# Performance work log

Measured on AMD Instinct MI355X. Metric: run time of the kernel, lower is better.

Reference implementation:

```python
import jax, jax.numpy as jnp
import numpy as np

B, L, D, H = 2, 2048, 1024, 16
HD = D // H  # head_dim = 64


def setup_inputs() -> dict:
    key = jax.random.key(0)
    ks = jax.random.split(key, 9)
    s = 0.02
    return {
        "x": jax.random.normal(ks[0], (B, L, D), dtype=jnp.float32),
        "wq": jax.random.normal(ks[1], (D, D), dtype=jnp.float32) * s,
        "bq": jnp.zeros((D,), dtype=jnp.float32),
        "wk": jax.random.normal(ks[2], (D, D), dtype=jnp.float32) * s,
        "bk": jnp.zeros((D,), dtype=jnp.float32),
        "wv": jax.random.normal(ks[3], (D, D), dtype=jnp.float32) * s,
        "bv": jnp.zeros((D,), dtype=jnp.float32),
        "wo": jax.random.normal(ks[4], (D, D), dtype=jnp.float32) * s,
        "bo": jnp.zeros((D,), dtype=jnp.float32),
    }


def reference(x, wq, bq, wk, bk, wv, bv, wo, bo):
    b, l, d = x.shape
    # projections -> [B, H, L, HD]
    def split_heads(t):
        return t.reshape(b, l, H, HD).transpose(0, 2, 1, 3)
    q = split_heads(x @ wq + bq)
    k = split_heads(x @ wk + bk)
    v = split_heads(x @ wv + bv)
    scores = jnp.einsum('bhqd,bhkd->bhqk', q, k) / jnp.sqrt(jnp.float32(HD))
    # causal mask via -inf then clamp to [-50, 50]: masked entries become -50 (faithful to torch code)
    mask = jnp.triu(jnp.full((l, l), -jnp.inf, dtype=scores.dtype), k=1)
    scores = jnp.clip(scores + mask[None, None, :, :], -50.0, 50.0)
    attn = jax.nn.softmax(scores, axis=-1)
    # dropout is identity in eval/deterministic mode
    out = jnp.einsum('bhqk,bhkd->bhqd', attn, v)
    out = out.transpose(0, 2, 1, 3).reshape(b, l, d)
    out = out @ wo + bo
    return out, attn
```

## Files before the change

kernel.cpp:

```cpp
#include <hip/hip_runtime.h>
#include <hip/hip_bf16.h>

#define B_  2
#define L_  2048
#define D_  1024
#define H_  16
#define HD_ 64

typedef __bf16 bf16x8 __attribute__((ext_vector_type(8)));
typedef float  f32x4  __attribute__((ext_vector_type(4)));
using bf16_t = __hip_bfloat16;

static __device__ __forceinline__ f32x4 mfma16(bf16x8 a, bf16x8 b, f32x4 c) {
    return __builtin_amdgcn_mfma_f32_16x16x32_bf16(a, b, c, 0, 0, 0);
}

static __device__ __forceinline__ void gl16(const bf16_t* g, bf16_t* l) {
    __builtin_amdgcn_global_load_lds(
        (const __attribute__((address_space(1))) unsigned int*)g,
        (__attribute__((address_space(3))) unsigned int*)l, 16, 0, 0);
}

__global__ __launch_bounds__(256) void k_convert(const float* __restrict__ in,
                                                 bf16_t* __restrict__ out, int n8) {
    int idx = blockIdx.x * 256 + threadIdx.x;
    if (idx >= n8) return;
    const float4* p = (const float4*)in + (size_t)idx * 2;
    float4 a = p[0], b = p[1];
    union { bf16_t h[8]; bf16x8 v; } u;
    u.h[0] = __float2bfloat16(a.x); u.h[1] = __float2bfloat16(a.y);
    u.h[2] = __float2bfloat16(a.z); u.h[3] = __float2bfloat16(a.w);
    u.h[4] = __float2bfloat16(b.x); u.h[5] = __float2bfloat16(b.y);
    u.h[6] = __float2bfloat16(b.z); u.h[7] = __float2bfloat16(b.w);
    *(bf16x8*)(out + (size_t)idx * 8) = u.v;
}

__global__ __launch_bounds__(256) void k_transpose4(
        const float* __restrict__ w0, const float* __restrict__ w1,
        const float* __restrict__ w2, const float* __restrict__ w3,
        bf16_t* __restrict__ t0, bf16_t* __restrict__ t1,
        bf16_t* __restrict__ t2, bf16_t* __restrict__ t3) {
    __shared__ bf16_t tile[64][65];
    int z = blockIdx.z;
    const float* w = (z == 0) ? w0 : (z == 1) ? w1 : (z == 2) ? w2 : w3;
    bf16_t* wt     = (z == 0) ? t0 : (z == 1) ? t1 : (z == 2) ? t2 : t3;
    int t  = threadIdx.x;
    int kb = blockIdx.x * 64, nb = blockIdx.y * 64;
    int r  = t >> 4, c4 = (t & 15) * 4;
    #pragma unroll
    for (int it = 0; it < 4; ++it) {
        int kr = r + it * 16;
        float4 v = *(const float4*)&w[(size_t)(kb + kr) * D_ + nb + c4];
        tile[kr][c4 + 0] = __float2bfloat16(v.x);
        tile[kr][c4 + 1] = __float2bfloat16(v.y);
        tile[kr][c4 + 2] = __float2bfloat16(v.z);
        tile[kr][c4 + 3] = __float2bfloat16(v.w);
    }
    __syncthreads();
    #pragma unroll
    for (int it = 0; it < 4; ++it) {
        int nr = r + it * 16;
        union { bf16_t h[4]; unsigned long long u; } o;
        o.h[0] = tile[c4 + 0][nr];
        o.h[1] = tile[c4 + 1][nr];
        o.h[2] = tile[c4 + 2][nr];
        o.h[3] = tile[c4 + 3][nr];
        *(unsigned long long*)&wt[(size_t)(nb + nr) * D_ + kb + c4] = o.u;
    }
}

__global__ __launch_bounds__(256, 3) void k_gemm_qkv(
        const bf16_t* __restrict__ A,
        const bf16_t* __restrict__ Wq, const bf16_t* __restrict__ Wk, const bf16_t* __restrict__ Wv,
        const float* __restrict__ bq, const float* __restrict__ bk, const float* __restrict__ bv,
        bf16_t* __restrict__ Qo, bf16_t* __restrict__ Ko, bf16_t* __restrict__ Vo) {
    __shared__ __align__(16) bf16_t Al[128][32];
    __shared__ __align__(16) bf16_t Bl[128][32];
    const int K = D_;
    int z = blockIdx.z;
    const bf16_t* Wt = (z == 0) ? Wq : (z == 1) ? Wk : Wv;
    const float* bias = (z == 0) ? bq : (z == 1) ? bk : bv;
    bf16_t* outp      = (z == 0) ? Qo : (z == 1) ? Ko : Vo;
    int tid = threadIdx.x, lane = tid & 63, wid = tid >> 6;
    int m0 = blockIdx.y * 128, n0 = blockIdx.x * 128;
    int wm = (wid >> 1) * 64, wn = (wid & 1) * 64;
    int r16 = lane & 15, g = lane >> 4;
    int lrow = lane >> 2, lcol = (lane & 3) * 8;
    f32x4 acc[4][4] = {};
    for (int kb = 0; kb < K; kb += 32) {
        __syncthreads();
        gl16(&A [(size_t)(m0 + wid * 32 + lrow) * K + kb + lcol],      &Al[wid * 32][0]);
        gl16(&A [(size_t)(m0 + wid * 32 + 16 + lrow) * K + kb + lcol], &Al[wid * 32 + 16][0]);
        gl16(&Wt[(size_t)(n0 + wid * 32 + lrow) * K + kb + lcol],      &Bl[wid * 32][0]);
        gl16(&Wt[(size_t)(n0 + wid * 32 + 16 + lrow) * K + kb + lcol], &Bl[wid * 32 + 16][0]);
        __syncthreads();
        bf16x8 af[4], bfr[4];
        #pragma unroll
        for (int i = 0; i < 4; ++i) af[i]  = *(const bf16x8*)&Al[wm + i * 16 + r16][g * 8];
        #pragma unroll
        for (int j = 0; j < 4; ++j) bfr[j] = *(const bf16x8*)&Bl[wn + j * 16 + r16][g * 8];
        #pragma unroll
        for (int i = 0; i < 4; ++i)
            #pragma unroll
            for (int j = 0; j < 4; ++j)
                acc[i][j] = mfma16(af[i], bfr[j], acc[i][j]);
    }
    #pragma unroll
    for (int i = 0; i < 4; ++i) {
        #pragma unroll
        for (int j = 0; j < 4; ++j) {
            int n = n0 + wn + j * 16 + r16;
            float bv2 = bias[n];
            #pragma unroll
            for (int e = 0; e < 4; ++e) {
                int m = m0 + wm + i * 16 + g * 4 + e;
                float v = acc[i][j][e] + bv2;
                int b = m >> 11, l = m & (L_ - 1);
                int h = n >> 6, hd = n & 63;
                if (z != 2)
                    outp[(((size_t)(b * H_ + h)) * L_ + l) * HD_ + hd] = __float2bfloat16(v);
                else
                    outp[(((size_t)(b * H_ + h)) * HD_ + hd) * L_ + l] = __float2bfloat16(v);
            }
        }
    }
}

__global__ __launch_bounds__(256, 2) void k_gemm_o(const bf16_t* __restrict__ A,
                                                   const bf16_t* __restrict__ Wt,
                                                   const float* __restrict__ bias,
                                                   float* __restrict__ outp) {
    __shared__ __align__(16) bf16_t Al[128][32];
    __shared__ __align__(16) bf16_t Bl[64][32];
    const int K = D_;
    int tid = threadIdx.x, lane = tid & 63, wid = tid >> 6;
    int m0 = blockIdx.y * 128, n0 = blockIdx.x * 64;
    int wm = (wid >> 1) * 64, wn = (wid & 1) * 32;
    int r16 = lane & 15, g = lane >> 4;
    int lrow = lane >> 2, lcol = (lane & 3) * 8;
    f32x4 acc[4][2] = {};
    for (int kb = 0; kb < K; kb += 32) {
        __syncthreads();
        gl16(&A [(size_t)(m0 + wid * 32 + lrow) * K + kb + lcol],      &Al[wid * 32][0]);
        gl16(&A [(size_t)(m0 + wid * 32 + 16 + lrow) * K + kb + lcol], &Al[wid * 32 + 16][0]);
        gl16(&Wt[(size_t)(n0 + wid * 16 + lrow) * K + kb + lcol],      &Bl[wid * 16][0]);
        __syncthreads();
        bf16x8 af[4], bfr[2];
        #pragma unroll
        for (int i = 0; i < 4; ++i) af[i]  = *(const bf16x8*)&Al[wm + i * 16 + r16][g * 8];
        #pragma unroll
        for (int j = 0; j < 2; ++j) bfr[j] = *(const bf16x8*)&Bl[wn + j * 16 + r16][g * 8];
        #pragma unroll
        for (int i = 0; i < 4; ++i)
            #pragma unroll
            for (int j = 0; j < 2; ++j)
                acc[i][j] = mfma16(af[i], bfr[j], acc[i][j]);
    }
    #pragma unroll
    for (int i = 0; i < 4; ++i)
        #pragma unroll
        for (int j = 0; j < 2; ++j) {
            int n = n0 + wn + j * 16 + r16;
            float bv = bias[n];
            #pragma unroll
            for (int e = 0; e < 4; ++e) {
                int m = m0 + wm + i * 16 + g * 4 + e;
                outp[(size_t)m * D_ + n] = acc[i][j][e] + bv;
            }
        }
}

__global__ __launch_bounds__(128, 3) void k_attn(const bf16_t* __restrict__ Q,
                                                 const bf16_t* __restrict__ Kb,
                                                 const bf16_t* __restrict__ VT,
                                                 bf16_t* __restrict__ ctx,
                                                 float* __restrict__ attn) {
    __shared__ __align__(16) bf16_t K_lds[2][32][64];
    __shared__ __align__(16) bf16_t V_lds[2][64][32];
    __shared__ __align__(16) char   pbuf[2][4608];

    int tid = threadIdx.x, lane = tid & 63, wid = tid >> 6;
    int bid = blockIdx.x;
    int j   = bid >> 3;
    int bh  = (bid & 7) + 8 * (j & 3);
    int qt64 = 31 - (j >> 2);
    int b = bh >> 4, h = bh & 15;
    int qb = qt64 * 64;
    const int diag = 2 * qt64 + 1;
    const bf16_t* Qh = Q  + (size_t)bh * L_ * HD_;
    const bf16_t* Kh = Kb + (size_t)bh * L_ * HD_;
    const bf16_t* Vh = VT + (size_t)bh * HD_ * L_;
    int r16 = lane & 15, g = lane >> 4;
    const float scale2 = 0.125f * 1.44269504088896340736f;
    const float clamp2 = 50.0f * 1.44269504088896340736f;

    bf16_t (*plds)[40] = (bf16_t(*)[40])pbuf[wid];
    float  (*pf32)[36] = (float (*)[36])pbuf[wid];

    int qrow0 = qb + wid * 32;

    bf16x8 q[2][2];
    #pragma unroll
    for (int p = 0; p < 2; ++p)
        #pragma unroll
        for (int hh = 0; hh < 2; ++hh)
            q[p][hh] = *(const bf16x8*)&Qh[(qrow0 + p * 16 + r16) * HD_ + hh * 32 + g * 8];

    int l = lane;
    int krow = l >> 3, kch = (l & 7) ^ (l >> 3);
    int vrow = l >> 2, vch = l & 3;
    auto STAGE_K = [&](int kt1, int nxt) {
        #pragma unroll
        for (int i = 0; i < 2; ++i) {
            int ii = wid * 2 + i;
            gl16(&Kh[(size_t)(kt1 * 32 + 8 * ii + krow) * 64 + kch * 8], &K_lds[nxt][8 * ii][0]);
        }
    };
    auto STAGE_V = [&](int kt1, int nxt) {
        #pragma unroll
        for (int i = 0; i < 2; ++i) {
            int ii = wid * 2 + i;
            gl16(&Vh[(size_t)(16 * ii + vrow) * L_ + kt1 * 32 + vch * 8], &V_lds[nxt][16 * ii][0]);
        }
    };

    f32x4 ctxa[2][4] = {};
    float zsum[2] = {0.f, 0.f};

    STAGE_K(0, 0); STAGE_V(0, 0);
    int cur = 0;
    for (int kt = 0; kt <= diag; ++kt) {
        __syncthreads();
        int nxt = cur ^ 1;
        if (kt < diag) { STAGE_K(kt + 1, nxt); STAGE_V(kt + 1, nxt); }
        bf16x8 kf[2][2], vf[4];
        #pragma unroll
        for (int s = 0; s < 2; ++s)
            #pragma unroll
            for (int hh = 0; hh < 2; ++hh)
                kf[s][hh] = *(const bf16x8*)&K_lds[cur][s * 16 + r16][((hh * 4 + g) ^ (r16 & 7)) * 8];
        #pragma unroll
        for (int t = 0; t < 4; ++t)
            vf[t] = *(const bf16x8*)&V_lds[cur][t * 16 + r16][g * 8];
        f32x4 sa[2][2];
        #pragma unroll
        for (int p = 0; p < 2; ++p)
            #pragma unroll
            for (int s = 0; s < 2; ++s) {
                f32x4 zz = {};
                sa[p][s] = mfma16(kf[s][1], q[p][1], mfma16(kf[s][0], q[p][0], zz));
            }
        int kb = kt * 32;
        #pragma unroll
        for (int p = 0; p < 2; ++p) {
            int qrow = qrow0 + p * 16 + r16;
            #pragma unroll
            for (int s = 0; s < 2; ++s) {
                union { bf16_t hv[4]; unsigned long long u; } pk;
                #pragma unroll
                for (int e = 0; e < 4; ++e) {
                    int key = kb + s * 16 + g * 4 + e;
                    float sc = sa[p][s][e] * scale2;
                    sc = fminf(fmaxf(sc, -clamp2), clamp2);
                    float ev = (key > qrow) ? 0.f : exp2f(sc);
                    zsum[p] += ev;
                    pk.hv[e] = __float2bfloat16(ev);
                }
                *(unsigned long long*)&plds[p * 16 + r16][s * 16 + g * 4] = pk.u;
            }
        }
        #pragma unroll
        for (int p = 0; p < 2; ++p) {
            bf16x8 pa = *(const bf16x8*)&plds[p * 16 + r16][g * 8];
            #pragma unroll
            for (int t = 0; t < 4; ++t)
                ctxa[p][t] = mfma16(pa, vf[t], ctxa[p][t]);
        }
        cur = nxt;
    }

    float invz[2];
    #pragma unroll
    for (int p = 0; p < 2; ++p) {
        float v = zsum[p];
        v += __shfl_xor(v, 16);
        v += __shfl_xor(v, 32);
        invz[p] = 1.f / v;
    }

    #pragma unroll
    for (int p = 0; p < 2; ++p) {
        #pragma unroll
        for (int e = 0; e < 4; ++e) {
            float izq = __shfl(invz[p], g * 4 + e);
            int qrow = qrow0 + p * 16 + g * 4 + e;
            #pragma unroll
            for (int t = 0; t < 4; ++t) {
                int col = h * HD_ + t * 16 + r16;
                ctx[((size_t)b * L_ + qrow) * D_ + col] =
                    __float2bfloat16(ctxa[p][t][e] * izq);
            }
        }
    }

    __syncthreads();
    STAGE_K(0, 0);
    cur = 0;
    for (int kt = 0; kt <= diag; ++kt) {
        __syncthreads();
        int nxt = cur ^ 1;
        if (kt < diag) STAGE_K(kt + 1, nxt);
        bf16x8 kf[2][2];
        #pragma unroll
        for (int s = 0; s < 2; ++s)
            #pragma unroll
            for (int hh = 0; hh < 2; ++hh)
                kf[s][hh] = *(const bf16x8*)&K_lds[cur][s * 16 + r16][((hh * 4 + g) ^ (r16 & 7)) * 8];
        f32x4 sa[2][2];
        #pragma unroll
        for (int p = 0; p < 2; ++p)
            #pragma unroll
            for (int s = 0; s < 2; ++s) {
                f32x4 zz = {};
                sa[p][s] = mfma16(kf[s][1], q[p][1], mfma16(kf[s][0], q[p][0], zz));
            }
        int kb = kt * 32;
        #pragma unroll
        for (int p = 0; p < 2; ++p) {
            int qrow = qrow0 + p * 16 + r16;
            #pragma unroll
            for (int s = 0; s < 2; ++s) {
                float4 fv;
                float* fp = &fv.x;
                #pragma unroll
                for (int e = 0; e < 4; ++e) {
                    int key = kb + s * 16 + g * 4 + e;
                    float sc = sa[p][s][e] * scale2;
                    sc = fminf(fmaxf(sc, -clamp2), clamp2);
                    fp[e] = (key > qrow) ? 0.f : exp2f(sc) * invz[p];
                }
                *(float4*)&pf32[p * 16 + r16][s * 16 + g * 4] = fv;
            }
        }
        #pragma unroll
        for (int jj = 0; jj < 4; ++jj) {
            int row = jj * 8 + (lane >> 3);
            float4 t = *(const float4*)&pf32[row][(lane & 7) * 4];
            *(float4*)&attn[((size_t)bh * L_ + qrow0 + row) * L_ + kb + (lane & 7) * 4] = t;
        }
        cur = nxt;
    }

    int zs = qb + 64;
    if (zs < L_) {
        float4 z4 = make_float4(0.f, 0.f, 0.f, 0.f);
        for (int r = 0; r < 32; ++r) {
            float* rowp = attn + ((size_t)bh * L_ + qrow0 + r) * L_;
            for (int c = zs + lane * 4; c < L_; c += 256)
                *(float4*)&rowp[c] = z4;
        }
    }
}

extern "C" void kernel_launch(void* const* d_in, const int* in_sizes, int n_in,
                              void* d_out, int out_size, void* d_ws, size_t ws_size,
                              hipStream_t stream) {
    const float* x  = (const float*)d_in[0];
    const float* wq = (const float*)d_in[1];
    const float* bq = (const float*)d_in[2];
    const float* wk = (const float*)d_in[3];
    const float* bk = (const float*)d_in[4];
    const float* wv = (const float*)d_in[5];
    const float* bv = (const float*)d_in[6];
    const float* wo = (const float*)d_in[7];
    const float* bo = (const float*)d_in[8];

    char* ws = (char*)d_ws;
    bf16_t* xb   = (bf16_t*)(ws);
    bf16_t* wqt  = (bf16_t*)(ws + ( 8u << 20));
    bf16_t* wkt  = (bf16_t*)(ws + (10u << 20));
    bf16_t* wvt  = (bf16_t*)(ws + (12u << 20));
    bf16_t* wot  = (bf16_t*)(ws + (14u << 20));
    bf16_t* Qb   = (bf16_t*)(ws + (16u << 20));
    bf16_t* Kbuf = (bf16_t*)(ws + (24u << 20));
    bf16_t* VTb  = (bf16_t*)(ws + (32u << 20));
    bf16_t* ctxb = (bf16_t*)(ws + (40u << 20));

    float* out  = (float*)d_out;
    float* attn = out + (size_t)B_ * L_ * D_;

    k_convert<<<2048, 256, 0, stream>>>(x, xb, (B_ * L_ * D_) / 8);
    dim3 tg4(16, 16, 4);
    k_transpose4<<<tg4, 256, 0, stream>>>(wq, wk, wv, wo, wqt, wkt, wvt, wot);

    dim3 g3(D_ / 128, (B_ * L_) / 128, 3);
    k_gemm_qkv<<<g3, 256, 0, stream>>>(xb, wqt, wkt, wvt, bq, bk, bv, Qb, Kbuf, VTb);

    k_attn<<<1024, 128, 0, stream>>>(Qb, Kbuf, VTb, ctxb, attn);

    dim3 gg(D_ / 64, (B_ * L_) / 128);
    k_gemm_o<<<gg, 256, 0, stream>>>(ctxb, wot, bo, (float*)d_out);
}
```

Measured before the change: 262.3 us.

## Restructure attention to 4-wave blocks with 64-key tiles and register-held P

Merges the x conversion and the weight transposes into one prep launch. Restructures the attention kernel so each block runs 4 waves of 16 query rows over 64-key K/V tiles. The softmax probabilities are packed into bf16 MFMA operands in registers with v_cvt_pk_bf16_f32, so they no longer go through an LDS scratch buffer. The V tile is swizzled to avoid bank conflicts, and attn rows are written straight from registers instead of being restaged through LDS. This cuts LDS traffic and barriers per tile, but the global stores of attn are less coalesced.

```diff
diff --git a/kernel.cpp b/kernel.cpp
--- a/kernel.cpp
+++ b/kernel.cpp
@@ -10,6 +10,8 @@
 typedef __bf16 bf16x8 __attribute__((ext_vector_type(8)));
 typedef float  f32x4  __attribute__((ext_vector_type(4)));
 using bf16_t = __hip_bfloat16;
+typedef unsigned int u32;
+typedef unsigned long long u64;
 
 static __device__ __forceinline__ f32x4 mfma16(bf16x8 a, bf16x8 b, f32x4 c) {
     return __builtin_amdgcn_mfma_f32_16x16x32_bf16(a, b, c, 0, 0, 0);
@@ -21,30 +23,38 @@
         (__attribute__((address_space(3))) unsigned int*)l, 16, 0, 0);
 }
 
-__global__ __launch_bounds__(256) void k_convert(const float* __restrict__ in,
-                                                 bf16_t* __restrict__ out, int n8) {
-    int idx = blockIdx.x * 256 + threadIdx.x;
-    if (idx >= n8) return;
-    const float4* p = (const float4*)in + (size_t)idx * 2;
-    float4 a = p[0], b = p[1];
-    union { bf16_t h[8]; bf16x8 v; } u;
-    u.h[0] = __float2bfloat16(a.x); u.h[1] = __float2bfloat16(a.y);
-    u.h[2] = __float2bfloat16(a.z); u.h[3] = __float2bfloat16(a.w);
-    u.h[4] = __float2bfloat16(b.x); u.h[5] = __float2bfloat16(b.y);
-    u.h[6] = __float2bfloat16(b.z); u.h[7] = __float2bfloat16(b.w);
-    *(bf16x8*)(out + (size_t)idx * 8) = u.v;
-}
-
-__global__ __launch_bounds__(256) void k_transpose4(
+static __device__ __forceinline__ u32 cvtpk(float lo, float hi) {
+    u32 r;
+    asm("v_cvt_pk_bf16_f32 %0, %1, %2" : "=v"(r) : "v"(lo), "v"(hi));
+    return r;
+}
+
+__global__ __launch_bounds__(256) void k_prep(
+        const float* __restrict__ x,
         const float* __restrict__ w0, const float* __restrict__ w1,
         const float* __restrict__ w2, const float* __restrict__ w3,
+        bf16_t* __restrict__ xb,
         bf16_t* __restrict__ t0, bf16_t* __restrict__ t1,
         bf16_t* __restrict__ t2, bf16_t* __restrict__ t3) {
     __shared__ bf16_t tile[64][65];
     int z = blockIdx.z;
+    int t = threadIdx.x;
+    if (z >= 4) {
+        int slice = z - 4;
+        int lin = blockIdx.y * 16 + blockIdx.x;
+        int idx = (slice * 256 + lin) * 256 + t;
+        const float4* p = (const float4*)x + (size_t)idx * 2;
+        float4 a = p[0], b = p[1];
+        union { bf16_t h[8]; bf16x8 v; } u;
+        u.h[0] = __float2bfloat16(a.x); u.h[1] = __float2bfloat16(a.y);
+        u.h[2] = __float2bfloat16(a.z); u.h[3] = __float2bfloat16(a.w);
+        u.h[4] = __float2bfloat16(b.x); u.h[5] = __float2bfloat16(b.y);
+        u.h[6] = __float2bfloat16(b.z); u.h[7] = __float2bfloat16(b.w);
+        *(bf16x8*)(xb + (size_t)idx * 8) = u.v;
+        return;
+    }
     const float* w = (z == 0) ? w0 : (z == 1) ? w1 : (z == 2) ? w2 : w3;
     bf16_t* wt     = (z == 0) ? t0 : (z == 1) ? t1 : (z == 2) ? t2 : t3;
-    int t  = threadIdx.x;
     int kb = blockIdx.x * 64, nb = blockIdx.y * 64;
     int r  = t >> 4, c4 = (t & 15) * 4;
     #pragma unroll
@@ -60,12 +70,12 @@
     #pragma unroll
     for (int it = 0; it < 4; ++it) {
         int nr = r + it * 16;
-        union { bf16_t h[4]; unsigned long long u; } o;
+        union { bf16_t h[4]; u64 u; } o;
         o.h[0] = tile[c4 + 0][nr];
         o.h[1] = tile[c4 + 1][nr];
         o.h[2] = tile[c4 + 2][nr];
         o.h[3] = tile[c4 + 3][nr];
-        *(unsigned long long*)&wt[(size_t)(nb + nr) * D_ + kb + c4] = o.u;
+        *(u64*)&wt[(size_t)(nb + nr) * D_ + kb + c4] = o.u;
     }
 }
 
@@ -170,62 +180,52 @@
         }
 }
 
-__global__ __launch_bounds__(128, 3) void k_attn(const bf16_t* __restrict__ Q,
+__global__ __launch_bounds__(256, 4) void k_attn(const bf16_t* __restrict__ Q,
                                                  const bf16_t* __restrict__ Kb,
                                                  const bf16_t* __restrict__ VT,
                                                  bf16_t* __restrict__ ctx,
                                                  float* __restrict__ attn) {
-    __shared__ __align__(16) bf16_t K_lds[2][32][64];
-    __shared__ __align__(16) bf16_t V_lds[2][64][32];
-    __shared__ __align__(16) char   pbuf[2][4608];
-
+    __shared__ __align__(16) bf16_t K_lds[2][64][64];
+    __shared__ __align__(16) bf16_t V_lds[2][64][64];
     int tid = threadIdx.x, lane = tid & 63, wid = tid >> 6;
     int bid = blockIdx.x;
-    int j   = bid >> 3;
-    int bh  = (bid & 7) + 8 * (j & 3);
-    int qt64 = 31 - (j >> 2);
+    int idx = bid >> 3;
+    int bh  = (bid & 7) + 8 * (idx & 3);
+    int qt  = 31 - (idx >> 2);
     int b = bh >> 4, h = bh & 15;
-    int qb = qt64 * 64;
-    const int diag = 2 * qt64 + 1;
+    int qb = qt * 64;
+    const int diag = qt;
     const bf16_t* Qh = Q  + (size_t)bh * L_ * HD_;
     const bf16_t* Kh = Kb + (size_t)bh * L_ * HD_;
     const bf16_t* Vh = VT + (size_t)bh * HD_ * L_;
     int r16 = lane & 15, g = lane >> 4;
     const float scale2 = 0.125f * 1.44269504088896340736f;
     const float clamp2 = 50.0f * 1.44269504088896340736f;
-
-    bf16_t (*plds)[40] = (bf16_t(*)[40])pbuf[wid];
-    float  (*pf32)[36] = (float (*)[36])pbuf[wid];
-
-    int qrow0 = qb + wid * 32;
-
-    bf16x8 q[2][2];
-    #pragma unroll
-    for (int p = 0; p < 2; ++p)
-        #pragma unroll
-        for (int hh = 0; hh < 2; ++hh)
-            q[p][hh] = *(const bf16x8*)&Qh[(qrow0 + p * 16 + r16) * HD_ + hh * 32 + g * 8];
-
-    int l = lane;
-    int krow = l >> 3, kch = (l & 7) ^ (l >> 3);
-    int vrow = l >> 2, vch = l & 3;
+    int qrow0 = qb + wid * 16;
+    int qrow  = qrow0 + r16;
+
+    bf16x8 q0 = *(const bf16x8*)&Qh[(size_t)(qrow0 + r16) * HD_ + g * 8];
+    bf16x8 q1 = *(const bf16x8*)&Qh[(size_t)(qrow0 + r16) * HD_ + 32 + g * 8];
+
+    int srow = lane >> 3, sunit = ((lane & 7) ^ (lane >> 3)) * 8;
     auto STAGE_K = [&](int kt1, int nxt) {
         #pragma unroll
         for (int i = 0; i < 2; ++i) {
-            int ii = wid * 2 + i;
-            gl16(&Kh[(size_t)(kt1 * 32 + 8 * ii + krow) * 64 + kch * 8], &K_lds[nxt][8 * ii][0]);
+            int cb = wid * 16 + i * 8;
+            gl16(&Kh[(size_t)(kt1 * 64 + cb + srow) * HD_ + sunit], &K_lds[nxt][cb][0]);
         }
     };
     auto STAGE_V = [&](int kt1, int nxt) {
         #pragma unroll
         for (int i = 0; i < 2; ++i) {
-            int ii = wid * 2 + i;
-            gl16(&Vh[(size_t)(16 * ii + vrow) * L_ + kt1 * 32 + vch * 8], &V_lds[nxt][16 * ii][0]);
+            int cb = wid * 16 + i * 8;
+            gl16(&Vh[(size_t)(cb + srow) * L_ + kt1 * 64 + sunit], &V_lds[nxt][cb][0]);
         }
     };
 
-    f32x4 ctxa[2][4] = {};
-    float zsum[2] = {0.f, 0.f};
+    f32x4 ctxa[4] = {};
+    float zsum = 0.f;
+    int rx = r16 & 7;
 
     STAGE_K(0, 0); STAGE_V(0, 0);
     int cur = 0;
@@ -233,128 +233,101 @@
         __syncthreads();
         int nxt = cur ^ 1;
         if (kt < diag) { STAGE_K(kt + 1, nxt); STAGE_V(kt + 1, nxt); }
-        bf16x8 kf[2][2], vf[4];
-        #pragma unroll
-        for (int s = 0; s < 2; ++s)
-            #pragma unroll
-            for (int hh = 0; hh < 2; ++hh)
-                kf[s][hh] = *(const bf16x8*)&K_lds[cur][s * 16 + r16][((hh * 4 + g) ^ (r16 & 7)) * 8];
-        #pragma unroll
-        for (int t = 0; t < 4; ++t)
-            vf[t] = *(const bf16x8*)&V_lds[cur][t * 16 + r16][g * 8];
-        f32x4 sa[2][2];
-        #pragma unroll
-        for (int p = 0; p < 2; ++p)
-            #pragma unroll
-            for (int s = 0; s < 2; ++s) {
+        int kb = kt * 64;
+        #pragma unroll
+        for (int sub = 0; sub < 2; ++sub) {
+            f32x4 sa[2];
+            #pragma unroll
+            for (int sp = 0; sp < 2; ++sp) {
+                int krow = sub * 32 + sp * 16 + r16;
+                bf16x8 kf0 = *(const bf16x8*)&K_lds[cur][krow][(g ^ rx) * 8];
+                bf16x8 kf1 = *(const bf16x8*)&K_lds[cur][krow][((4 + g) ^ rx) * 8];
                 f32x4 zz = {};
-                sa[p][s] = mfma16(kf[s][1], q[p][1], mfma16(kf[s][0], q[p][0], zz));
-            }
-        int kb = kt * 32;
-        #pragma unroll
-        for (int p = 0; p < 2; ++p) {
-            int qrow = qrow0 + p * 16 + r16;
-            #pragma unroll
-            for (int s = 0; s < 2; ++s) {
-                union { bf16_t hv[4]; unsigned long long u; } pk;
+                sa[sp] = mfma16(kf1, q1, mfma16(kf0, q0, zz));
+            }
+            int kb2 = kb + sub * 32;
+            u32 dw[2][2];
+            #pragma unroll
+            for (int sp = 0; sp < 2; ++sp) {
+                float ev[4];
                 #pragma unroll
                 for (int e = 0; e < 4; ++e) {
-                    int key = kb + s * 16 + g * 4 + e;
-                    float sc = sa[p][s][e] * scale2;
-                    sc = fminf(fmaxf(sc, -clamp2), clamp2);
-                    float ev = (key > qrow) ? 0.f : exp2f(sc);
-                    zsum[p] += ev;
-                    pk.hv[e] = __float2bfloat16(ev);
+                    int key = kb2 + sp * 16 + g * 4 + e;
+                    float sc = fminf(fmaxf(sa[sp][e] * scale2, -clamp2), clamp2);
+                    ev[e] = (key > qrow) ? 0.f : exp2f(sc);
+                    zsum += ev[e];
                 }
-                *(unsigned long long*)&plds[p * 16 + r16][s * 16 + g * 4] = pk.u;
-            }
-        }
-        #pragma unroll
-        for (int p = 0; p < 2; ++p) {
-            bf16x8 pa = *(const bf16x8*)&plds[p * 16 + r16][g * 8];
-            #pragma unroll
-            for (int t = 0; t < 4; ++t)
-                ctxa[p][t] = mfma16(pa, vf[t], ctxa[p][t]);
+                dw[sp][0] = cvtpk(ev[0], ev[1]);
+                dw[sp][1] = cvtpk(ev[2], ev[3]);
+            }
+            union { u32 u[4]; bf16x8 v; } pa;
+            pa.u[0] = dw[0][0]; pa.u[1] = dw[0][1];
+            pa.u[2] = dw[1][0]; pa.u[3] = dw[1][1];
+            #pragma unroll
+            for (int t = 0; t < 4; ++t) {
+                int vrow = t * 16 + r16;
+                int u0 = ((sub * 4 + (g >> 1)) ^ rx) * 8 + (g & 1) * 4;
+                int u1 = ((sub * 4 + 2 + (g >> 1)) ^ rx) * 8 + (g & 1) * 4;
+                union { u64 d[2]; bf16x8 v; } vf;
+                vf.d[0] = *(const u64*)&V_lds[cur][vrow][u0];
+                vf.d[1] = *(const u64*)&V_lds[cur][vrow][u1];
+                ctxa[t] = mfma16(pa.v, vf.v, ctxa[t]);
+            }
         }
         cur = nxt;
-    }
-
-    float invz[2];
-    #pragma unroll
-    for (int p = 0; p < 2; ++p) {
-        float v = zsum[p];
-        v += __shfl_xor(v, 16);
-        v += __shfl_xor(v, 32);
-        invz[p] = 1.f / v;
-    }
-
-    #pragma unroll
-    for (int p = 0; p < 2; ++p) {
-        #pragma unroll
-        for (int e = 0; e < 4; ++e) {
-            float izq = __shfl(invz[p], g * 4 + e);
-            int qrow = qrow0 + p * 16 + g * 4 + e;
-            #pragma unroll
-            for (int t = 0; t < 4; ++t) {
-                int col = h * HD_ + t * 16 + r16;
-                ctx[((size_t)b * L_ + qrow) * D_ + col] =
-                    __float2bfloat16(ctxa[p][t][e] * izq);
-            }
-        }
     }
 
     __syncthreads();
     STAGE_K(0, 0);
+
+    float v = zsum;
+    v += __shfl_xor(v, 16);
+    v += __shfl_xor(v, 32);
+    float invz = 1.f / v;
+
+    #pragma unroll
+    for (int e = 0; e < 4; ++e) {
+        float izq = __shfl(invz, g * 4 + e);
+        int qr = qrow0 + g * 4 + e;
+        #pragma unroll
+        for (int t = 0; t < 4; ++t)
+            ctx[((size_t)b * L_ + qr) * D_ + h * HD_ + t * 16 + r16] =
+                __float2bfloat16(ctxa[t][e] * izq);
+    }
+
     cur = 0;
     for (int kt = 0; kt <= diag; ++kt) {
         __syncthreads();
         int nxt = cur ^ 1;
         if (kt < diag) STAGE_K(kt + 1, nxt);
-        bf16x8 kf[2][2];
-        #pragma unroll
-        for (int s = 0; s < 2; ++s)
-            #pragma unroll
-            for (int hh = 0; hh < 2; ++hh)
-                kf[s][hh] = *(const bf16x8*)&K_lds[cur][s * 16 + r16][((hh * 4 + g) ^ (r16 & 7)) * 8];
-        f32x4 sa[2][2];
-        #pragma unroll
-        for (int p = 0; p < 2; ++p)
-            #pragma unroll
-            for (int s = 0; s < 2; ++s) {
+        int kb = kt * 64;
+        #pragma unroll
+        for (int sub = 0; sub < 2; ++sub)
+            #pragma unroll
+            for (int sp = 0; sp < 2; ++sp) {
+                int krow = sub * 32 + sp * 16 + r16;
+                bf16x8 kf0 = *(const bf16x8*)&K_lds[cur][krow][(g ^ rx) * 8];
+                bf16x8 kf1 = *(const bf16x8*)&K_lds[cur][krow][((4 + g) ^ rx) * 8];
                 f32x4 zz = {};
-                sa[p][s] = mfma16(kf[s][1], q[p][1], mfma16(kf[s][0], q[p][0], zz));
-            }
-        int kb = kt * 32;
-        #pragma unroll
-        for (int p = 0; p < 2; ++p) {
-            int qrow = qrow0 + p * 16 + r16;
-            #pragma unroll
-            for (int s = 0; s < 2; ++s) {
+                f32x4 sa = mfma16(kf1, q1, mfma16(kf0, q0, zz));
+                int cb = kb + sub * 32 + sp * 16 + g * 4;
                 float4 fv;
                 float* fp = &fv.x;
                 #pragma unroll
                 for (int e = 0; e < 4; ++e) {
-                    int key = kb + s * 16 + g * 4 + e;
-                    float sc = sa[p][s][e] * scale2;
-                    sc = fminf(fmaxf(sc, -clamp2), clamp2);
-                    fp[e] = (key > qrow) ? 0.f : exp2f(sc) * invz[p];
+                    int key = cb + e;
+                    float sc = fminf(fmaxf(sa[e] * scale2, -clamp2), clamp2);
+                    fp[e] = (key > qrow) ? 0.f : exp2f(sc) * invz;
                 }
-                *(float4*)&pf32[p * 16 + r16][s * 16 + g * 4] = fv;
-            }
-        }
-        #pragma unroll
-        for (int jj = 0; jj < 4; ++jj) {
-            int row = jj * 8 + (lane >> 3);
-            float4 t = *(const float4*)&pf32[row][(lane & 7) * 4];
-            *(float4*)&attn[((size_t)bh * L_ + qrow0 + row) * L_ + kb + (lane & 7) * 4] = t;
-        }
+                *(float4*)&attn[((size_t)bh * L_ + qrow) * L_ + cb] = fv;
+            }
         cur = nxt;
     }
 
     int zs = qb + 64;
     if (zs < L_) {
         float4 z4 = make_float4(0.f, 0.f, 0.f, 0.f);
-        for (int r = 0; r < 32; ++r) {
+        for (int r = 0; r < 16; ++r) {
             float* rowp = attn + ((size_t)bh * L_ + qrow0 + r) * L_;
             for (int c = zs + lane * 4; c < L_; c += 256)
                 *(float4*)&rowp[c] = z4;
@@ -389,14 +362,13 @@
     float* out  = (float*)d_out;
     float* attn = out + (size_t)B_ * L_ * D_;
 
-    k_convert<<<2048, 256, 0, stream>>>(x, xb, (B_ * L_ * D_) / 8);
-    dim3 tg4(16, 16, 4);
-    k_transpose4<<<tg4, 256, 0, stream>>>(wq, wk, wv, wo, wqt, wkt, wvt, wot);
+    dim3 gp(16, 16, 12);
+    k_prep<<<gp, 256, 0, stream>>>(x, wq, wk, wv, wo, xb, wqt, wkt, wvt, wot);
 
     dim3 g3(D_ / 128, (B_ * L_) / 128, 3);
     k_gemm_qkv<<<g3, 256, 0, stream>>>(xb, wqt, wkt, wvt, bq, bk, bv, Qb, Kbuf, VTb);
 
-    k_attn<<<1024, 128, 0, stream>>>(Qb, Kbuf, VTb, ctxb, attn);
+    k_attn<<<1024, 256, 0, stream>>>(Qb, Kbuf, VTb, ctxb, attn);
 
     dim3 gg(D_ / 64, (B_ * L_) / 128);
     k_gemm_o<<<gg, 256, 0, stream>>>(ctxb, wot, bo, (float*)d_out);
```

After: 267.5 us. Within noise of the previous version (+2.0%).
